# Kernel tuning notes

Measured on AMD Instinct MI355X. Metric: run time of the kernel, lower is better.

## Reference

```python
import jax, jax.numpy as jnp
import numpy as np

NUM_CLASSES = 21
TOP_K = 200
CONF_THRESH = 0.01
NMS_THRESH = 0.045
VAR0, VAR1 = 0.1, 0.2  # SSD decode variances
B, N = 128, 8732  # batch, num anchors (SSD300)


def setup_inputs() -> dict:
    key = jax.random.key(0)
    k1, k2, k3 = jax.random.split(key, 3)
    loc = jax.random.normal(k1, (B, N, 4), jnp.float32)
    conf = jax.random.normal(k2, (B, N, NUM_CLASSES), jnp.float32)
    # anchors in center-size form (cx, cy, w, h), values in (0,1)
    anchors = jax.random.uniform(k3, (N, 4), jnp.float32)
    return {"loc": loc, "conf": conf, "anchors": anchors}


def decode(loc, anchors):
    # loc [N,4], anchors [N,4] (cx,cy,w,h) -> corner boxes [N,4]
    cxcy = anchors[:, :2] + loc[:, :2] * VAR0 * anchors[:, 2:]
    wh = anchors[:, 2:] * jnp.exp(loc[:, 2:] * VAR1)
    return jnp.concatenate([cxcy - 0.5 * wh, cxcy + 0.5 * wh], axis=-1)


def pairwise_iou(boxes):
    # boxes [K,4] -> IoU [K,K]
    lt = jnp.maximum(boxes[:, None, :2], boxes[None, :, :2])
    rb = jnp.minimum(boxes[:, None, 2:], boxes[None, :, 2:])
    wh = jnp.clip(rb - lt, 0.0)
    inter = wh[..., 0] * wh[..., 1]
    area = (boxes[:, 2] - boxes[:, 0]) * (boxes[:, 3] - boxes[:, 1])
    return inter / (area[:, None] + area[None, :] - inter + 1e-12)


def nms_one_class(scores, boxes):
    # scores [N], boxes [N,4] -> packed [TOP_K, 5] (score, x1,y1,x2,y2)
    masked = jnp.where(scores > CONF_THRESH, scores, 0.0)
    top_s, idx = jax.lax.top_k(masked, TOP_K)
    top_b = boxes[idx]                      # [K,4]
    iou = pairwise_iou(top_b)               # [K,K]
    ar = jnp.arange(TOP_K)
    def body(i, keep):
        sup = keep[i] & (iou[i] > NMS_THRESH) & (ar > i)
        return keep & ~sup
    keep = jax.lax.fori_loop(0, TOP_K, body, top_s > CONF_THRESH)
    # pack kept detections to the front (stable sort preserves score order)
    order = jnp.argsort(jnp.logical_not(keep))
    ent = jnp.concatenate([top_s[:, None], top_b], axis=-1)[order]
    return jnp.where(keep[order][:, None], ent, 0.0)


def reference(loc, conf, anchors):
    probs = jax.nn.softmax(conf, axis=-1)   # [B,N,C]
    def per_image(loc_i, probs_i):
        boxes = decode(loc_i, anchors)      # [N,4]
        return jax.vmap(lambda s: nms_one_class(s, boxes))(probs_i.T)  # [C,K,5]
    out = jax.vmap(per_image)(loc, probs)   # [B,C,K,5]
    return out.at[:, 0].set(0.0)            # class 0 = background, left zero
```

## Files before the change

### kernel.cpp

```cpp
#include <hip/hip_runtime.h>
#include <math.h>

#pragma clang fp contract(off)

#define NB 128
#define NA 8732
#define NC 21
#define TOPK 200
#define BCAP 512
#define CONF_T 0.01
#define NMS_T 0.045
#define NQ (NA / 4)
#define HSIZE 904
#define CHN 226
#define CHPAD 232
#define CH2N 29

__device__ __forceinline__ double exact_score_cf(const float* __restrict__ conf,
                                                 int b, int i, int c) {
  const float* row = conf + ((size_t)b * NA + i) * NC;
  float r[NC];
#pragma unroll
  for (int k = 0; k < NC; ++k) r[k] = row[k];
  float mx = r[0];
#pragma unroll
  for (int k = 1; k < NC; ++k) mx = fmaxf(mx, r[k]);
  double d = 0.0;
#pragma unroll
  for (int k = 0; k < NC; ++k) d += exp((double)r[k] - (double)mx);
  double s = exp((double)r[c] - (double)mx) / d;
  return (s > CONF_T) ? s : 0.0;
}

__device__ __forceinline__ double exact_score_aux(const float* __restrict__ conf,
                                                  const float* __restrict__ mxa,
                                                  const double* __restrict__ da,
                                                  int b, int i, int c) {
  size_t r = (size_t)b * NA + i;
  double v = (double)conf[r * NC + c];
  double m = (double)mxa[r];
  double s = exp(v - m) / da[r];
  return (s > CONF_T) ? s : 0.0;
}

__device__ __forceinline__ double exact_score(const float* __restrict__ conf,
                                              const float* __restrict__ mxa,
                                              const double* __restrict__ da,
                                              int use_aux, int b, int i, int c) {
  if (use_aux) return exact_score_aux(conf, mxa, da, b, i, c);
  return exact_score_cf(conf, b, i, c);
}

__device__ __forceinline__ void decode64(const float* __restrict__ loc,
                                         const float* __restrict__ anchors,
                                         int b, int ai, double* o) {
  const float* lp = loc + ((size_t)b * NA + ai) * 4;
  const float* ap = anchors + (size_t)ai * 4;
  double l0 = (double)lp[0], l1 = (double)lp[1];
  double l2 = (double)lp[2], l3 = (double)lp[3];
  double a0 = (double)ap[0], a1 = (double)ap[1];
  double a2 = (double)ap[2], a3 = (double)ap[3];
  double cx = a0 + (l0 * 0.1) * a2;
  double cy = a1 + (l1 * 0.1) * a3;
  double w = a2 * exp(l2 * 0.2);
  double h = a3 * exp(l3 * 0.2);
  o[0] = cx - 0.5 * w; o[1] = cy - 0.5 * h;
  o[2] = cx + 0.5 * w; o[3] = cy + 0.5 * h;
}

__device__ __forceinline__ bool entBefore(double sa, int ia, double sb, int ib) {
  return (sa > sb) || (sa == sb && ia < ib);
}

__device__ __forceinline__ int kbucket(unsigned key) {
  if (key == 0u) return -1;
  int x = (int)(key >> 16) - 0x3C00 + 1;
  if (x < 1) x = 1;
  if (x > HSIZE - 1) x = HSIZE - 1;
  return x;
}

__global__ __launch_bounds__(256) void k_prep(const float* __restrict__ conf,
                                              float* __restrict__ scores,
                                              float* __restrict__ mxout,
                                              double* __restrict__ dout,
                                              int do_aux) {
  __shared__ float rows[256 * NC];
  int base = blockIdx.x * 256;
  const float4* src = (const float4*)(conf + (size_t)base * NC);
  float4* dst = (float4*)rows;
  for (int t = threadIdx.x; t < (256 * NC) / 4; t += 256) dst[t] = src[t];
  __syncthreads();
  int g = base + threadIdx.x;
  const float* row = rows + threadIdx.x * NC;
  float v[NC];
#pragma unroll
  for (int k = 0; k < NC; ++k) v[k] = row[k];
  float mx = v[0];
#pragma unroll
  for (int k = 1; k < NC; ++k) mx = fmaxf(mx, v[k]);
  float e[NC], s = 0.0f;
#pragma unroll
  for (int k = 0; k < NC; ++k) {
    e[k] = expf(v[k] - mx);
    s += e[k];
  }
  float inv = 1.0f / s;
  int b = g / NA, i = g - b * NA;
#pragma unroll
  for (int cc = 1; cc < NC; ++cc) {
    float sc = e[cc] * inv;
    scores[(size_t)(b * (NC - 1) + (cc - 1)) * NA + i] = (sc > 0.0099f) ? sc : 0.0f;
  }
  if (do_aux) {
    double d = 0.0;
#pragma unroll
    for (int k = 0; k < NC; ++k) d += exp((double)v[k] - (double)mx);
    mxout[g] = mx;
    dout[g] = d;
  }
}

__global__ __launch_bounds__(256, 8) void k_fast(const float* __restrict__ loc,
                                                 const float* __restrict__ conf,
                                                 const float* __restrict__ anchors,
                                                 const float* __restrict__ scores,
                                                 const float* __restrict__ mxa,
                                                 const double* __restrict__ da,
                                                 float* __restrict__ out,
                                                 int use_aux) {
  int id = blockIdx.x;
  int xcd = id & 7, slot0 = id >> 3;
  int c = slot0 % NC;
  int b = (slot0 / NC) * 8 + xcd;
  int tid = threadIdx.x;
  float* outbase = out + ((size_t)(b * NC + c)) * TOPK * 5;

  if (c == 0) {
    for (int k = tid; k < TOPK * 5; k += 256) outbase[k] = 0.0f;
    return;
  }

  __shared__ unsigned hist[HSIZE];
  __shared__ unsigned chunk[CHPAD];
  __shared__ unsigned chunk2[32];
  union U2 {
    struct { double bnds[BCAP]; int bndi[BCAP]; } bb;
    double dbox[TOPK][4];
  };
  __shared__ U2 u2;
  union U3 {
    unsigned suf[HSIZE];
    struct { float4 fbox[TOPK]; float farea[TOPK]; } fb;
  };
  __shared__ U3 u3;
  __shared__ double ssel[256];
  __shared__ int isel[256];
  __shared__ unsigned keepw[7];
  __shared__ int ctl_cnt, ctl_m, ctl_n1, ctl_kneed, ctl_lo, ctl_hi, ctl_k, ctl_fix;
  __shared__ unsigned ctl_pref;

  const float4* sc4 =
      (const float4*)(scores + (size_t)(b * (NC - 1) + (c - 1)) * NA);

  for (int t = tid; t < HSIZE; t += 256) hist[t] = 0u;
  for (int t = tid; t < TOPK; t += 256) isel[t] = 0;
  if (tid == 0) { ctl_cnt = 0; ctl_m = 0; ctl_fix = 0; }
  __syncthreads();

  for (int q = tid; q < NQ; q += 256) {
    float4 k4 = sc4[q];
    unsigned kb[4] = {__float_as_uint(k4.x), __float_as_uint(k4.y),
                      __float_as_uint(k4.z), __float_as_uint(k4.w)};
#pragma unroll
    for (int t = 0; t < 4; ++t) {
      int idx = kbucket(kb[t]);
      if (idx >= 0) atomicAdd(&hist[idx], 1u);
    }
  }
  __syncthreads();

  if (tid < CHN) {
    unsigned csum = 0;
#pragma unroll
    for (int j = 0; j < 4; ++j) csum += hist[tid * 4 + j];
    chunk[tid] = csum;
  } else if (tid < CHPAD) {
    chunk[tid] = 0u;
  }
  __syncthreads();

  if (tid < CH2N) {
    unsigned s = 0;
#pragma unroll
    for (int j = 0; j < 8; ++j) s += chunk[tid * 8 + j];
    chunk2[tid] = s;
  }
  __syncthreads();

  if (tid == 0) {
    unsigned cum = 0;
    int t2 = -1;
    for (int t = CH2N - 1; t >= 0; --t) {
      unsigned h = chunk2[t];
      if (cum + h >= (unsigned)TOPK) { t2 = t; break; }
      cum += h;
    }
    if (t2 < 0) {
      ctl_lo = 1; ctl_hi = 0; ctl_n1 = (int)cum; ctl_kneed = TOPK - (int)cum;
    } else {
      int tc = t2 * 8;
      for (int t = t2 * 8 + 7; t >= t2 * 8; --t) {
        unsigned h = chunk[t];
        if (cum + h >= (unsigned)TOPK) { tc = t; break; }
        cum += h;
      }
      int D = tc * 4;
      for (int j = tc * 4 + 3; j >= tc * 4; --j) {
        unsigned h = hist[j];
        if (cum + h >= (unsigned)TOPK) { D = j; break; }
        cum += h;
      }
      int hi = (D + 1 < HSIZE) ? D + 1 : D;
      int lo = (D - 1 >= 1) ? D - 1 : D;
      unsigned hup = (hi > D) ? hist[hi] : 0u;
      ctl_lo = lo; ctl_hi = hi;
      ctl_n1 = (int)(cum - hup);
      ctl_kneed = TOPK - ctl_n1;
    }
    unsigned run = 0;
    for (int w = CH2N - 1; w >= 0; --w) {
      unsigned h = chunk2[w];
      chunk2[w] = run;
      run += h;
    }
  }
  __syncthreads();
  int lo = ctl_lo, hi = ctl_hi, n1 = ctl_n1, kneed = ctl_kneed;

  if (tid < CHN) {
    unsigned s = chunk2[tid >> 3];
    int ge = ((tid >> 3) + 1) << 3;
    for (int u = tid + 1; u < ge; ++u) s += chunk[u];
    int b0 = tid * 4;
    unsigned h3 = hist[b0 + 3], h2 = hist[b0 + 2], h1 = hist[b0 + 1];
    u3.suf[b0 + 3] = s;
    u3.suf[b0 + 2] = s + h3;
    u3.suf[b0 + 1] = s + h3 + h2;
    u3.suf[b0 + 0] = s + h3 + h2 + h1;
  }
  __syncthreads();

  for (int t = tid; t < HSIZE; t += 256) hist[t] = 0u;
  __syncthreads();

  {
    unsigned tCert = (unsigned)(0x3C00 + hi) << 16;
    unsigned tBnd = (unsigned)(0x3BFF + lo) << 16;
    for (int q = tid; q < NQ; q += 256) {
      float4 k4 = sc4[q];
      unsigned kb[4] = {__float_as_uint(k4.x), __float_as_uint(k4.y),
                        __float_as_uint(k4.z), __float_as_uint(k4.w)};
#pragma unroll
      for (int t = 0; t < 4; ++t) {
        unsigned key = kb[t];
        if (key >= tCert) {
          int bk = kbucket(key);
          int slot = (int)u3.suf[bk] + (int)atomicAdd(&hist[bk], 1u);
          if (slot < TOPK) isel[slot] = (bk << 16) | (q * 4 + t);
        } else if (key >= tBnd) {
          int p = atomicAdd(&ctl_m, 1);
          if (p < BCAP) u2.bb.bndi[p] = q * 4 + t;
        }
      }
    }
  }
  __syncthreads();
  int m = (hi > 0) ? ctl_m : 0;

  if (hi > 0 && m > BCAP) {
    if (tid == 0) { ctl_k = TOPK; ctl_pref = 0u; }
    __syncthreads();
    for (int shift = 24; shift >= 0; shift -= 8) {
      hist[tid] = 0u;
      __syncthreads();
      unsigned pref = ctl_pref;
      for (int q = tid; q < NQ; q += 256) {
        float4 k4 = sc4[q];
        unsigned kb[4] = {__float_as_uint(k4.x), __float_as_uint(k4.y),
                          __float_as_uint(k4.z), __float_as_uint(k4.w)};
#pragma unroll
        for (int t = 0; t < 4; ++t) {
          unsigned key = kb[t];
          if (key == 0u) continue;
          bool match = (shift == 24) || ((key >> (shift + 8)) == (pref >> (shift + 8)));
          if (match) atomicAdd(&hist[(key >> shift) & 255u], 1u);
        }
      }
      __syncthreads();
      if (tid == 0) {
        int k = ctl_k;
        unsigned cum = 0;
        int d = 255;
        for (; d > 0; --d) {
          unsigned h = hist[d];
          if (cum + h >= (unsigned)k) break;
          cum += h;
        }
        ctl_k = k - (int)cum;
        ctl_pref = pref | ((unsigned)d << shift);
      }
      __syncthreads();
    }
    unsigned Tf = ctl_pref;
    kneed = ctl_k;
    n1 = TOPK - kneed;
    if (tid == 0) { ctl_cnt = 0; ctl_m = 0; }
    __syncthreads();
    for (int q = tid; q < NQ; q += 256) {
      float4 k4 = sc4[q];
      unsigned kb[4] = {__float_as_uint(k4.x), __float_as_uint(k4.y),
                        __float_as_uint(k4.z), __float_as_uint(k4.w)};
#pragma unroll
      for (int t = 0; t < 4; ++t) {
        unsigned key = kb[t];
        if (key > Tf) {
          int p = atomicAdd(&ctl_cnt, 1);
          if (p < 256) isel[p] = q * 4 + t;
        } else if (key == Tf) {
          int p = atomicAdd(&ctl_m, 1);
          if (p < BCAP) u2.bb.bndi[p] = q * 4 + t;
        }
      }
    }
    __syncthreads();
    m = ctl_m;
    if (m > BCAP) m = BCAP;
    for (int q = tid; q < m; q += 256)
      u2.bb.bnds[q] = exact_score(conf, mxa, da, use_aux, b, u2.bb.bndi[q], c);
    __syncthreads();
    for (int q = tid; q < m; q += 256) {
      double sq = u2.bb.bnds[q];
      int iq = u2.bb.bndi[q];
      int rank = 0;
      for (int r = 0; r < m; ++r)
        if (entBefore(u2.bb.bnds[r], u2.bb.bndi[r], sq, iq)) ++rank;
      if (rank < kneed) { isel[n1 + rank] = iq; ssel[n1 + rank] = sq; }
    }
    __syncthreads();
    if (tid < TOPK) {
      if (tid < n1) ssel[tid] = exact_score(conf, mxa, da, use_aux, b, isel[tid], c);
    } else {
      ssel[tid] = -1.0;
      isel[tid] = 0x7fffffff;
    }
    for (int kk = 2; kk <= 256; kk <<= 1) {
      for (int j = kk >> 1; j > 0; j >>= 1) {
        __syncthreads();
        int ixj = tid ^ j;
        if (ixj > tid) {
          double s1 = ssel[tid], s2 = ssel[ixj];
          int i1 = isel[tid], i2 = isel[ixj];
          bool up = ((tid & kk) == 0);
          bool sw = up ? entBefore(s2, i2, s1, i1) : entBefore(s1, i1, s2, i2);
          if (sw) {
            ssel[tid] = s2; ssel[ixj] = s1;
            isel[tid] = i2; isel[ixj] = i1;
          }
        }
      }
    }
    __syncthreads();
  } else {
    if (tid < n1)
      ssel[tid] = exact_score(conf, mxa, da, use_aux, b, isel[tid] & 0xFFFF, c);
    if (hi > 0) {
      for (int q = tid; q < m; q += 256)
        u2.bb.bnds[q] = exact_score(conf, mxa, da, use_aux, b, u2.bb.bndi[q], c);
    }
    __syncthreads();
    double myS = 0.0;
    int myI = 0, myPos = -1;
    if (tid < n1) {
      int packed = isel[tid];
      int bk = packed >> 16;
      myI = packed & 0xFFFF;
      myS = ssel[tid];
      int base = (int)u3.suf[bk];
      int len = (int)u3.suf[bk - 1] - base;
      int r = 0;
      for (int u = base; u < base + len; ++u) {
        if (u == tid) continue;
        double ps = ssel[u];
        int pI = isel[u] & 0xFFFF;
        if (entBefore(ps, pI, myS, myI)) ++r;
      }
      myPos = base + r;
    }
    if (hi > 0) {
      for (int q = tid; q < m; q += 256) {
        double sq = u2.bb.bnds[q];
        int iq = u2.bb.bndi[q];
        int rank = 0;
        for (int r = 0; r < m; ++r)
          if (entBefore(u2.bb.bnds[r], u2.bb.bndi[r], sq, iq)) ++rank;
        if (rank < kneed) { isel[n1 + rank] = iq; ssel[n1 + rank] = sq; }
      }
    } else {
      for (int j = n1 + tid; j < TOPK; j += 256) {
        isel[j] = j - n1;
        ssel[j] = 0.0;
      }
    }
    __syncthreads();
    if (myPos >= 0 && myPos < TOPK) { ssel[myPos] = myS; isel[myPos] = myI; }
    __syncthreads();
    if (tid < 64) {
      bool inv = false;
      for (int j = tid + 1; j < TOPK; j += 64)
        if (entBefore(ssel[j], isel[j], ssel[j - 1], isel[j - 1])) inv = true;
      unsigned long long bal = __ballot((int)inv);
      if (tid == 0 && bal != 0ull) ctl_fix = 1;
    }
    __syncthreads();
    if (ctl_fix) {
      if (tid == 0) {
        for (int a = 1; a < TOPK; ++a) {
          double s = ssel[a];
          int ii = isel[a];
          int p = a - 1;
          while (p >= 0 && entBefore(s, ii, ssel[p], isel[p])) {
            ssel[p + 1] = ssel[p]; isel[p + 1] = isel[p]; --p;
          }
          ssel[p + 1] = s; isel[p + 1] = ii;
        }
      }
      __syncthreads();
    }
  }

  double dx1 = 0, dy1 = 0, dx2 = 0, dy2 = 0;
  if (tid < TOPK) {
    double bx[4];
    decode64(loc, anchors, b, isel[tid], bx);
    dx1 = bx[0]; dy1 = bx[1]; dx2 = bx[2]; dy2 = bx[3];
    u3.fb.fbox[tid] = make_float4((float)dx1, (float)dy1, (float)dx2, (float)dy2);
    u3.fb.farea[tid] = (float)((dx2 - dx1) * (dy2 - dy1));
    u2.dbox[tid][0] = dx1; u2.dbox[tid][1] = dy1;
    u2.dbox[tid][2] = dx2; u2.dbox[tid][3] = dy2;
  }
  __syncthreads();

  if (tid < 64) {
    int l = tid;
    unsigned kr = 0u;
    float4 ob[4]; float oa[4];
#pragma unroll
    for (int q = 0; q < 4; ++q) {
      int j = l + 64 * q;
      if (j < TOPK) {
        if (ssel[j] > CONF_T) kr |= 1u << q;
        ob[q] = u3.fb.fbox[j];
        oa[q] = u3.fb.farea[j];
      } else {
        ob[q] = make_float4(0.0f, 0.0f, 0.0f, 0.0f);
        oa[q] = 0.0f;
      }
    }
    int cur = 0;
    while (cur < TOPK) {
      unsigned long long ms0 = __ballot((int)(kr & 1u));
      unsigned long long ms1 = __ballot((int)(kr & 2u));
      unsigned long long ms2 = __ballot((int)(kr & 4u));
      unsigned long long ms3 = __ballot((int)(kr & 8u));
      int q0 = cur >> 6;
      int sh = cur & 63;
      unsigned long long below = sh ? ((1ull << sh) - 1ull) : 0ull;
      unsigned long long t0 = (q0 == 0) ? (ms0 & ~below) : 0ull;
      unsigned long long t1 = (q0 < 1) ? ms1 : ((q0 == 1) ? (ms1 & ~below) : 0ull);
      unsigned long long t2 = (q0 < 2) ? ms2 : ((q0 == 2) ? (ms2 & ~below) : 0ull);
      unsigned long long t3 = (q0 < 3) ? ms3 : (ms3 & ~below);
      int i = TOPK;
      if (t0) i = __ffsll(t0) - 1;
      else if (t1) i = 64 + __ffsll(t1) - 1;
      else if (t2) i = 128 + __ffsll(t2) - 1;
      else if (t3) i = 192 + __ffsll(t3) - 1;
      if (i >= TOPK) break;
      float4 fbi = u3.fb.fbox[i];
      float fai = u3.fb.farea[i];
#pragma unroll
      for (int q = 0; q < 4; ++q) {
        int r = l + 64 * q;
        if (r > i && r < TOPK && ((kr >> q) & 1u)) {
          float lx = fmaxf(fbi.x, ob[q].x), ly = fmaxf(fbi.y, ob[q].y);
          float rx = fminf(fbi.z, ob[q].z), ry = fminf(fbi.w, ob[q].w);
          float iw = fmaxf(rx - lx, 0.0f), ih = fmaxf(ry - ly, 0.0f);
          float inter = iw * ih;
          float uni = fai + oa[q] - inter + 1e-12f;
          float diff = inter - 0.045f * uni;
          bool sup;
          if (fabsf(diff) < 3e-4f * uni) {
            double ix1 = u2.dbox[i][0], iy1 = u2.dbox[i][1];
            double ix2 = u2.dbox[i][2], iy2 = u2.dbox[i][3];
            double jx1 = u2.dbox[r][0], jy1 = u2.dbox[r][1];
            double jx2 = u2.dbox[r][2], jy2 = u2.dbox[r][3];
            double dlx = fmax(ix1, jx1), dly = fmax(iy1, jy1);
            double drx = fmin(ix2, jx2), dry = fmin(iy2, jy2);
            double diw = drx - dlx; if (diw < 0.0) diw = 0.0;
            double dih = dry - dly; if (dih < 0.0) dih = 0.0;
            double dint = diw * dih;
            double dai = (ix2 - ix1) * (iy2 - iy1);
            double daj = (jx2 - jx1) * (jy2 - jy1);
            sup = dint > NMS_T * (dai + daj - dint + 1e-12);
          } else {
            sup = diff > 0.0f;
          }
          if (sup) kr &= ~(1u << q);
        }
      }
      cur = i + 1;
    }
#pragma unroll
    for (int q = 0; q < 4; ++q) {
      unsigned long long bal = __ballot((int)((kr >> q) & 1u));
      if (l == 0) {
        keepw[2 * q] = (unsigned)bal;
        if (2 * q + 1 < 7) keepw[2 * q + 1] = (unsigned)(bal >> 32);
      }
    }
  }
  __syncthreads();

  int nk = 0;
#pragma unroll
  for (int w = 0; w < 7; ++w) nk += __popc(keepw[w]);
  if (tid < TOPK) {
    int j = tid;
    bool kept = (keepw[j >> 5] >> (j & 31)) & 1u;
    if (kept) {
      int pos = 0;
      for (int w = 0; w < (j >> 5); ++w) pos += __popc(keepw[w]);
      pos += __popc(keepw[j >> 5] & ((1u << (j & 31)) - 1u));
      float* o = outbase + (size_t)pos * 5;
      o[0] = (float)ssel[j];
      o[1] = (float)dx1;
      o[2] = (float)dy1;
      o[3] = (float)dx2;
      o[4] = (float)dy2;
    }
    if (j >= nk) {
      float* o = outbase + (size_t)j * 5;
      o[0] = 0.0f; o[1] = 0.0f; o[2] = 0.0f; o[3] = 0.0f; o[4] = 0.0f;
    }
  }
}

__global__ __launch_bounds__(256) void k_main_nf(const float* __restrict__ loc,
                                                 const float* __restrict__ conf,
                                                 const float* __restrict__ anchors,
                                                 float* __restrict__ out) {
  int bc = blockIdx.x;
  int b = bc / NC;
  int c = bc % NC;
  int tid = threadIdx.x;
  float* outbase = out + (size_t)bc * TOPK * 5;
  if (c == 0) {
    for (int k = tid; k < TOPK * 5; k += 256) outbase[k] = 0.0f;
    return;
  }
  union U {
    float sf[NA];
    struct { double box[TOPK][4]; double area[TOPK]; } p2;
  };
  __shared__ U u;
  __shared__ double ssel[256];
  __shared__ int isel[256];
  __shared__ unsigned hist[256];
  __shared__ double bnds[256];
  __shared__ int bndi[256];
  __shared__ int keepL[256];
  __shared__ unsigned long long wmask[4];
  __shared__ int ctl_k, ctl_cnt, ctl_m;
  __shared__ unsigned ctl_pref;

  for (int i = tid; i < NA; i += 256)
    u.sf[i] = (float)exact_score_cf(conf, b, i, c);
  if (tid == 0) { ctl_k = TOPK; ctl_pref = 0u; }
  __syncthreads();
  for (int shift = 24; shift >= 0; shift -= 8) {
    hist[tid] = 0u;
    __syncthreads();
    unsigned pref = ctl_pref;
    for (int i = tid; i < NA; i += 256) {
      unsigned key = __float_as_uint(u.sf[i]);
      bool match = (shift == 24) || ((key >> (shift + 8)) == (pref >> (shift + 8)));
      if (match) atomicAdd(&hist[(key >> shift) & 255u], 1u);
    }
    __syncthreads();
    if (tid == 0) {
      int k = ctl_k;
      unsigned cum = 0;
      int d = 255;
      for (; d > 0; --d) {
        unsigned h = hist[d];
        if (cum + h >= (unsigned)k) break;
        cum += h;
      }
      ctl_k = k - (int)cum;
      ctl_pref = pref | ((unsigned)d << shift);
    }
    __syncthreads();
  }
  unsigned Tf = ctl_pref;
  int kneed = ctl_k;
  int n1 = TOPK - kneed;
  if (tid == 0) { ctl_cnt = 0; ctl_m = 0; }
  __syncthreads();
  for (int i = tid; i < NA; i += 256) {
    unsigned key = __float_as_uint(u.sf[i]);
    if (key > Tf) {
      int p = atomicAdd(&ctl_cnt, 1);
      if (p < 256) isel[p] = i;
    } else if (key == Tf && Tf != 0u) {
      int q = atomicAdd(&ctl_m, 1);
      if (q < 256) bndi[q] = i;
    }
  }
  __syncthreads();
  int zf;
  if (Tf == 0u) {
    zf = n1;
    for (int j = n1 + tid; j < TOPK; j += 256) isel[j] = j - n1;
  } else {
    zf = TOPK;
    int m = ctl_m;
    if (m > 256) m = 256;
    if (tid < m) bnds[tid] = exact_score_cf(conf, b, bndi[tid], c);
    __syncthreads();
    if (tid < m) {
      double sq = bnds[tid];
      int iq = bndi[tid];
      int rank = 0;
      for (int r = 0; r < m; ++r)
        if (entBefore(bnds[r], bndi[r], sq, iq)) ++rank;
      if (rank < kneed) isel[n1 + rank] = iq;
    }
  }
  __syncthreads();
  if (tid < TOPK) {
    ssel[tid] = (tid < zf) ? exact_score_cf(conf, b, isel[tid], c) : 0.0;
  } else {
    ssel[tid] = -1.0;
    isel[tid] = 0x7fffffff;
  }
  for (int kk = 2; kk <= 256; kk <<= 1) {
    for (int j = kk >> 1; j > 0; j >>= 1) {
      __syncthreads();
      int ixj = tid ^ j;
      if (ixj > tid) {
        double s1 = ssel[tid], s2 = ssel[ixj];
        int i1 = isel[tid], i2 = isel[ixj];
        bool up = ((tid & kk) == 0);
        bool sw = up ? entBefore(s2, i2, s1, i1) : entBefore(s1, i1, s2, i2);
        if (sw) {
          ssel[tid] = s2; ssel[ixj] = s1;
          isel[tid] = i2; isel[ixj] = i1;
        }
      }
    }
  }
  __syncthreads();
  if (tid < TOPK) {
    double bx[4];
    decode64(loc, anchors, b, isel[tid], bx);
    u.p2.box[tid][0] = bx[0]; u.p2.box[tid][1] = bx[1];
    u.p2.box[tid][2] = bx[2]; u.p2.box[tid][3] = bx[3];
    u.p2.area[tid] = (bx[2] - bx[0]) * (bx[3] - bx[1]);
  }
  __syncthreads();
  double mx1 = 0, my1 = 0, mx2 = 0, my2 = 0, mar = 0;
  if (tid < TOPK) {
    mx1 = u.p2.box[tid][0]; my1 = u.p2.box[tid][1];
    mx2 = u.p2.box[tid][2]; my2 = u.p2.box[tid][3];
    mar = u.p2.area[tid];
  }
  keepL[tid] = (tid < TOPK) && (ssel[tid] > CONF_T);
  __syncthreads();
  for (int i = 0; i < TOPK; ++i) {
    int ki = keepL[i];
    if (ki && tid > i && tid < TOPK && keepL[tid]) {
      double lx = fmax(u.p2.box[i][0], mx1);
      double ly = fmax(u.p2.box[i][1], my1);
      double rx = fmin(u.p2.box[i][2], mx2);
      double ry = fmin(u.p2.box[i][3], my2);
      double iw = rx - lx; if (iw < 0.0) iw = 0.0;
      double ih = ry - ly; if (ih < 0.0) ih = 0.0;
      double inter = iw * ih;
      double iou = inter / (u.p2.area[i] + mar - inter + 1e-12);
      if (iou > NMS_T) keepL[tid] = 0;
    }
    __syncthreads();
  }
  bool kj = (tid < TOPK) && (keepL[tid] != 0);
  unsigned long long bal = __ballot((int)kj);
  int wave = tid >> 6, lane = tid & 63;
  if (lane == 0) wmask[wave] = bal;
  __syncthreads();
  int nk = 0;
#pragma unroll
  for (int w = 0; w < 4; ++w) nk += __popcll(wmask[w]);
  if (kj) {
    int pos = 0;
    for (int w = 0; w < wave; ++w) pos += __popcll(wmask[w]);
    pos += __popcll(bal & ((1ull << lane) - 1ull));
    float* o = outbase + (size_t)pos * 5;
    o[0] = (float)ssel[tid];
    o[1] = (float)u.p2.box[tid][0];
    o[2] = (float)u.p2.box[tid][1];
    o[3] = (float)u.p2.box[tid][2];
    o[4] = (float)u.p2.box[tid][3];
  }
  if (tid < TOPK && tid >= nk) {
    float* o = outbase + (size_t)tid * 5;
    o[0] = 0.0f; o[1] = 0.0f; o[2] = 0.0f; o[3] = 0.0f; o[4] = 0.0f;
  }
}

extern "C" void kernel_launch(void* const* d_in, const int* in_sizes, int n_in,
                              void* d_out, int out_size, void* d_ws, size_t ws_size,
                              hipStream_t stream) {
  const float* loc = (const float*)d_in[0];
  const float* conf = (const float*)d_in[1];
  const float* anchors = (const float*)d_in[2];
  float* out = (float*)d_out;

  const size_t SC_BYTES = (size_t)NB * (NC - 1) * NA * sizeof(float);
  const size_t MX_BYTES = (size_t)NB * NA * sizeof(float);
  const size_t D_BYTES = (size_t)NB * NA * sizeof(double);

  if (ws_size >= SC_BYTES + MX_BYTES + D_BYTES) {
    float* scores = (float*)d_ws;
    float* mxa = (float*)((char*)d_ws + SC_BYTES);
    double* da = (double*)((char*)d_ws + SC_BYTES + MX_BYTES);
    k_prep<<<(NB * NA) / 256, 256, 0, stream>>>(conf, scores, mxa, da, 1);
    k_fast<<<NB * NC, 256, 0, stream>>>(loc, conf, anchors, scores, mxa, da, out, 1);
  } else if (ws_size >= SC_BYTES) {
    float* scores = (float*)d_ws;
    k_prep<<<(NB * NA) / 256, 256, 0, stream>>>(conf, scores, nullptr, nullptr, 0);
    k_fast<<<NB * NC, 256, 0, stream>>>(loc, conf, anchors, scores, nullptr, nullptr, out, 0);
  } else {
    k_main_nf<<<NB * NC, 256, 0, stream>>>(loc, conf, anchors, out);
  }
}
```

Baseline: 119.8 us.

## Store truncated 16-bit score keys and prefilter histogram with sampled threshold

k_prep now writes only the upper 16 bits of each float score into a padded bf16-like key array, which halves the intermediate score traffic. k_fast reads eight keys per 16-byte load. It first samples 256 keys to estimate a lower bound, so the first histogram pass only does atomics for keys above that bound, and it reruns the pass without the bound if fewer than TOPK keys are found. The radix refinement shrinks to two 8-bit passes over the 16-bit keys, with exact double scores still used for boundary ties. A small extra kernel zeroes the row padding, which adds one launch per call.

```diff
diff --git a/kernel.cpp b/kernel.cpp
--- a/kernel.cpp
+++ b/kernel.cpp
@@ -5,16 +5,18 @@
 
 #define NB 128
 #define NA 8732
+#define NAP 8736
 #define NC 21
 #define TOPK 200
 #define BCAP 512
 #define CONF_T 0.01
 #define NMS_T 0.045
-#define NQ (NA / 4)
+#define NV (NAP / 8)
 #define HSIZE 904
 #define CHN 226
 #define CHPAD 232
 #define CH2N 29
+#define KSAMP 30
 
 __device__ __forceinline__ double exact_score_cf(const float* __restrict__ conf,
                                                  int b, int i, int c) {
@@ -72,16 +74,8 @@
   return (sa > sb) || (sa == sb && ia < ib);
 }
 
-__device__ __forceinline__ int kbucket(unsigned key) {
-  if (key == 0u) return -1;
-  int x = (int)(key >> 16) - 0x3C00 + 1;
-  if (x < 1) x = 1;
-  if (x > HSIZE - 1) x = HSIZE - 1;
-  return x;
-}
-
 __global__ __launch_bounds__(256) void k_prep(const float* __restrict__ conf,
-                                              float* __restrict__ scores,
+                                              unsigned short* __restrict__ scores,
                                               float* __restrict__ mxout,
                                               double* __restrict__ dout,
                                               int do_aux) {
@@ -110,7 +104,9 @@
 #pragma unroll
   for (int cc = 1; cc < NC; ++cc) {
     float sc = e[cc] * inv;
-    scores[(size_t)(b * (NC - 1) + (cc - 1)) * NA + i] = (sc > 0.0099f) ? sc : 0.0f;
+    scores[(size_t)(b * (NC - 1) + (cc - 1)) * NAP + i] =
+        (sc > 0.0099f) ? (unsigned short)(__float_as_uint(sc) >> 16)
+                       : (unsigned short)0;
   }
   if (do_aux) {
     double d = 0.0;
@@ -121,10 +117,18 @@
   }
 }
 
+__global__ __launch_bounds__(256) void k_pad(unsigned short* __restrict__ scores) {
+  int r = blockIdx.x * 256 + threadIdx.x;
+  if (r < NB * (NC - 1)) {
+    unsigned short* p = scores + (size_t)r * NAP + NA;
+    p[0] = 0; p[1] = 0; p[2] = 0; p[3] = 0;
+  }
+}
+
 __global__ __launch_bounds__(256, 8) void k_fast(const float* __restrict__ loc,
                                                  const float* __restrict__ conf,
                                                  const float* __restrict__ anchors,
-                                                 const float* __restrict__ scores,
+                                                 const unsigned short* __restrict__ scores,
                                                  const float* __restrict__ mxa,
                                                  const double* __restrict__ da,
                                                  float* __restrict__ out,
@@ -157,86 +161,123 @@
   __shared__ double ssel[256];
   __shared__ int isel[256];
   __shared__ unsigned keepw[7];
-  __shared__ int ctl_cnt, ctl_m, ctl_n1, ctl_kneed, ctl_lo, ctl_hi, ctl_k, ctl_fix;
-  __shared__ unsigned ctl_pref;
-
-  const float4* sc4 =
-      (const float4*)(scores + (size_t)(b * (NC - 1) + (c - 1)) * NA);
-
-  for (int t = tid; t < HSIZE; t += 256) hist[t] = 0u;
+  __shared__ int ctl_cnt, ctl_m, ctl_n1, ctl_kneed, ctl_lo, ctl_hi, ctl_k;
+  __shared__ int ctl_fix, ctl_redo;
+  __shared__ unsigned ctl_pref, ctl_L;
+
+  const unsigned short* srow =
+      scores + (size_t)(b * (NC - 1) + (c - 1)) * NAP;
+  const uint4* sv = (const uint4*)srow;
+
   for (int t = tid; t < TOPK; t += 256) isel[t] = 0;
+  if (tid < 32) chunk2[tid] = 0u;
   if (tid == 0) { ctl_cnt = 0; ctl_m = 0; ctl_fix = 0; }
   __syncthreads();
-
-  for (int q = tid; q < NQ; q += 256) {
-    float4 k4 = sc4[q];
-    unsigned kb[4] = {__float_as_uint(k4.x), __float_as_uint(k4.y),
-                      __float_as_uint(k4.z), __float_as_uint(k4.w)};
-#pragma unroll
-    for (int t = 0; t < 4; ++t) {
-      int idx = kbucket(kb[t]);
-      if (idx >= 0) atomicAdd(&hist[idx], 1u);
-    }
-  }
-  __syncthreads();
-
-  if (tid < CHN) {
-    unsigned csum = 0;
-#pragma unroll
-    for (int j = 0; j < 4; ++j) csum += hist[tid * 4 + j];
-    chunk[tid] = csum;
-  } else if (tid < CHPAD) {
-    chunk[tid] = 0u;
-  }
-  __syncthreads();
-
-  if (tid < CH2N) {
-    unsigned s = 0;
-#pragma unroll
-    for (int j = 0; j < 8; ++j) s += chunk[tid * 8 + j];
-    chunk2[tid] = s;
-  }
-  __syncthreads();
-
+  {
+    unsigned k16 = srow[tid * 34];
+    if (k16) {
+      int x = (int)k16 - 0x3BFF;
+      if (x < 1) x = 1;
+      if (x > HSIZE - 1) x = HSIZE - 1;
+      atomicAdd(&chunk2[x >> 5], 1u);
+    }
+  }
+  __syncthreads();
   if (tid == 0) {
     unsigned cum = 0;
-    int t2 = -1;
+    int w = -1;
     for (int t = CH2N - 1; t >= 0; --t) {
-      unsigned h = chunk2[t];
-      if (cum + h >= (unsigned)TOPK) { t2 = t; break; }
-      cum += h;
-    }
-    if (t2 < 0) {
-      ctl_lo = 1; ctl_hi = 0; ctl_n1 = (int)cum; ctl_kneed = TOPK - (int)cum;
-    } else {
-      int tc = t2 * 8;
-      for (int t = t2 * 8 + 7; t >= t2 * 8; --t) {
-        unsigned h = chunk[t];
-        if (cum + h >= (unsigned)TOPK) { tc = t; break; }
+      cum += chunk2[t];
+      if (cum >= (unsigned)KSAMP) { w = t; break; }
+    }
+    ctl_L = (w >= 1) ? (unsigned)(0x3BFF + (w << 5)) : 0u;
+  }
+  __syncthreads();
+
+  unsigned L16x = ctl_L ? ctl_L : 1u;
+  int lo, hi, n1, kneed;
+  for (;;) {
+    for (int t = tid; t < HSIZE; t += 256) hist[t] = 0u;
+    if (tid == 0) ctl_redo = 0;
+    __syncthreads();
+    for (int q = tid; q < NV; q += 256) {
+      uint4 v = sv[q];
+      unsigned ks[8] = {v.x & 0xFFFFu, v.x >> 16, v.y & 0xFFFFu, v.y >> 16,
+                        v.z & 0xFFFFu, v.z >> 16, v.w & 0xFFFFu, v.w >> 16};
+#pragma unroll
+      for (int t = 0; t < 8; ++t) {
+        if (ks[t] >= L16x) {
+          int x = (int)ks[t] - 0x3BFF;
+          if (x < 1) x = 1;
+          if (x > HSIZE - 1) x = HSIZE - 1;
+          atomicAdd(&hist[x], 1u);
+        }
+      }
+    }
+    __syncthreads();
+    if (tid < CHN) {
+      unsigned csum = 0;
+#pragma unroll
+      for (int j = 0; j < 4; ++j) csum += hist[tid * 4 + j];
+      chunk[tid] = csum;
+    } else if (tid < CHPAD) {
+      chunk[tid] = 0u;
+    }
+    __syncthreads();
+    if (tid < CH2N) {
+      unsigned s = 0;
+#pragma unroll
+      for (int j = 0; j < 8; ++j) s += chunk[tid * 8 + j];
+      chunk2[tid] = s;
+    }
+    if (tid >= CH2N && tid < 32) chunk2[tid] = 0u;
+    __syncthreads();
+    if (tid == 0) {
+      unsigned cum = 0;
+      int t2 = -1;
+      for (int t = CH2N - 1; t >= 0; --t) {
+        unsigned h = chunk2[t];
+        if (cum + h >= (unsigned)TOPK) { t2 = t; break; }
         cum += h;
       }
-      int D = tc * 4;
-      for (int j = tc * 4 + 3; j >= tc * 4; --j) {
-        unsigned h = hist[j];
-        if (cum + h >= (unsigned)TOPK) { D = j; break; }
-        cum += h;
-      }
-      int hi = (D + 1 < HSIZE) ? D + 1 : D;
-      int lo = (D - 1 >= 1) ? D - 1 : D;
-      unsigned hup = (hi > D) ? hist[hi] : 0u;
-      ctl_lo = lo; ctl_hi = hi;
-      ctl_n1 = (int)(cum - hup);
-      ctl_kneed = TOPK - ctl_n1;
-    }
-    unsigned run = 0;
-    for (int w = CH2N - 1; w >= 0; --w) {
-      unsigned h = chunk2[w];
-      chunk2[w] = run;
-      run += h;
-    }
-  }
-  __syncthreads();
-  int lo = ctl_lo, hi = ctl_hi, n1 = ctl_n1, kneed = ctl_kneed;
+      if (t2 < 0 && L16x > 1u) {
+        ctl_redo = 1;
+      } else {
+        if (t2 < 0) {
+          ctl_lo = 1; ctl_hi = 0; ctl_n1 = (int)cum; ctl_kneed = TOPK - (int)cum;
+        } else {
+          int tc = t2 * 8;
+          for (int t = t2 * 8 + 7; t >= t2 * 8; --t) {
+            unsigned h = chunk[t];
+            if (cum + h >= (unsigned)TOPK) { tc = t; break; }
+            cum += h;
+          }
+          int D = tc * 4;
+          for (int j = tc * 4 + 3; j >= tc * 4; --j) {
+            unsigned h = hist[j];
+            if (cum + h >= (unsigned)TOPK) { D = j; break; }
+            cum += h;
+          }
+          int hi_ = (D + 1 < HSIZE) ? D + 1 : D;
+          int lo_ = (D - 1 >= 1) ? D - 1 : D;
+          unsigned hup = (hi_ > D) ? hist[hi_] : 0u;
+          ctl_lo = lo_; ctl_hi = hi_;
+          ctl_n1 = (int)(cum - hup);
+          ctl_kneed = TOPK - ctl_n1;
+        }
+        unsigned run = 0;
+        for (int w = CH2N - 1; w >= 0; --w) {
+          unsigned h = chunk2[w];
+          chunk2[w] = run;
+          run += h;
+        }
+      }
+    }
+    __syncthreads();
+    if (!ctl_redo) break;
+    L16x = 1u;
+  }
+  lo = ctl_lo; hi = ctl_hi; n1 = ctl_n1; kneed = ctl_kneed;
 
   if (tid < CHN) {
     unsigned s = chunk2[tid >> 3];
@@ -255,22 +296,23 @@
   __syncthreads();
 
   {
-    unsigned tCert = (unsigned)(0x3C00 + hi) << 16;
-    unsigned tBnd = (unsigned)(0x3BFF + lo) << 16;
-    for (int q = tid; q < NQ; q += 256) {
-      float4 k4 = sc4[q];
-      unsigned kb[4] = {__float_as_uint(k4.x), __float_as_uint(k4.y),
-                        __float_as_uint(k4.z), __float_as_uint(k4.w)};
-#pragma unroll
-      for (int t = 0; t < 4; ++t) {
-        unsigned key = kb[t];
-        if (key >= tCert) {
-          int bk = kbucket(key);
-          int slot = (int)u3.suf[bk] + (int)atomicAdd(&hist[bk], 1u);
-          if (slot < TOPK) isel[slot] = (bk << 16) | (q * 4 + t);
-        } else if (key >= tBnd) {
+    unsigned tC16 = (unsigned)(0x3C00 + hi);
+    unsigned tB16 = (unsigned)(0x3BFF + lo);
+    for (int q = tid; q < NV; q += 256) {
+      uint4 v = sv[q];
+      unsigned ks[8] = {v.x & 0xFFFFu, v.x >> 16, v.y & 0xFFFFu, v.y >> 16,
+                        v.z & 0xFFFFu, v.z >> 16, v.w & 0xFFFFu, v.w >> 16};
+#pragma unroll
+      for (int t = 0; t < 8; ++t) {
+        unsigned key = ks[t];
+        if (key >= tC16) {
+          int x = (int)key - 0x3BFF;
+          if (x > HSIZE - 1) x = HSIZE - 1;
+          int slot = (int)u3.suf[x] + (int)atomicAdd(&hist[x], 1u);
+          if (slot < TOPK) isel[slot] = (x << 16) | (q * 8 + t);
+        } else if (key >= tB16) {
           int p = atomicAdd(&ctl_m, 1);
-          if (p < BCAP) u2.bb.bndi[p] = q * 4 + t;
+          if (p < BCAP) u2.bb.bndi[p] = q * 8 + t;
         }
       }
     }
@@ -281,19 +323,19 @@
   if (hi > 0 && m > BCAP) {
     if (tid == 0) { ctl_k = TOPK; ctl_pref = 0u; }
     __syncthreads();
-    for (int shift = 24; shift >= 0; shift -= 8) {
+    for (int shift = 8; shift >= 0; shift -= 8) {
       hist[tid] = 0u;
       __syncthreads();
       unsigned pref = ctl_pref;
-      for (int q = tid; q < NQ; q += 256) {
-        float4 k4 = sc4[q];
-        unsigned kb[4] = {__float_as_uint(k4.x), __float_as_uint(k4.y),
-                          __float_as_uint(k4.z), __float_as_uint(k4.w)};
-#pragma unroll
-        for (int t = 0; t < 4; ++t) {
-          unsigned key = kb[t];
+      for (int q = tid; q < NV; q += 256) {
+        uint4 v = sv[q];
+        unsigned ks[8] = {v.x & 0xFFFFu, v.x >> 16, v.y & 0xFFFFu, v.y >> 16,
+                          v.z & 0xFFFFu, v.z >> 16, v.w & 0xFFFFu, v.w >> 16};
+#pragma unroll
+        for (int t = 0; t < 8; ++t) {
+          unsigned key = ks[t];
           if (key == 0u) continue;
-          bool match = (shift == 24) || ((key >> (shift + 8)) == (pref >> (shift + 8)));
+          bool match = (shift == 8) || ((key >> 8) == (pref >> 8));
           if (match) atomicAdd(&hist[(key >> shift) & 255u], 1u);
         }
       }
@@ -317,19 +359,19 @@
     n1 = TOPK - kneed;
     if (tid == 0) { ctl_cnt = 0; ctl_m = 0; }
     __syncthreads();
-    for (int q = tid; q < NQ; q += 256) {
-      float4 k4 = sc4[q];
-      unsigned kb[4] = {__float_as_uint(k4.x), __float_as_uint(k4.y),
-                        __float_as_uint(k4.z), __float_as_uint(k4.w)};
-#pragma unroll
-      for (int t = 0; t < 4; ++t) {
-        unsigned key = kb[t];
+    for (int q = tid; q < NV; q += 256) {
+      uint4 v = sv[q];
+      unsigned ks[8] = {v.x & 0xFFFFu, v.x >> 16, v.y & 0xFFFFu, v.y >> 16,
+                        v.z & 0xFFFFu, v.z >> 16, v.w & 0xFFFFu, v.w >> 16};
+#pragma unroll
+      for (int t = 0; t < 8; ++t) {
+        unsigned key = ks[t];
         if (key > Tf) {
           int p = atomicAdd(&ctl_cnt, 1);
-          if (p < 256) isel[p] = q * 4 + t;
+          if (p < 256) isel[p] = q * 8 + t;
         } else if (key == Tf) {
           int p = atomicAdd(&ctl_m, 1);
-          if (p < BCAP) u2.bb.bndi[p] = q * 4 + t;
+          if (p < BCAP) u2.bb.bndi[p] = q * 8 + t;
         }
       }
     }
@@ -734,18 +776,20 @@
   const float* anchors = (const float*)d_in[2];
   float* out = (float*)d_out;
 
-  const size_t SC_BYTES = (size_t)NB * (NC - 1) * NA * sizeof(float);
+  const size_t SC_BYTES = (size_t)NB * (NC - 1) * NAP * sizeof(unsigned short);
   const size_t MX_BYTES = (size_t)NB * NA * sizeof(float);
   const size_t D_BYTES = (size_t)NB * NA * sizeof(double);
 
   if (ws_size >= SC_BYTES + MX_BYTES + D_BYTES) {
-    float* scores = (float*)d_ws;
+    unsigned short* scores = (unsigned short*)d_ws;
     float* mxa = (float*)((char*)d_ws + SC_BYTES);
     double* da = (double*)((char*)d_ws + SC_BYTES + MX_BYTES);
+    k_pad<<<10, 256, 0, stream>>>(scores);
     k_prep<<<(NB * NA) / 256, 256, 0, stream>>>(conf, scores, mxa, da, 1);
     k_fast<<<NB * NC, 256, 0, stream>>>(loc, conf, anchors, scores, mxa, da, out, 1);
   } else if (ws_size >= SC_BYTES) {
-    float* scores = (float*)d_ws;
+    unsigned short* scores = (unsigned short*)d_ws;
+    k_pad<<<10, 256, 0, stream>>>(scores);
     k_prep<<<(NB * NA) / 256, 256, 0, stream>>>(conf, scores, nullptr, nullptr, 0);
     k_fast<<<NB * NC, 256, 0, stream>>>(loc, conf, anchors, scores, nullptr, nullptr, out, 0);
   } else {
```

Measured after the change: 116.9 us. 2.4% less time.
